# Kernel optimization log

Measured on AMD Instinct MI355X. Metric: run time of the kernel, lower is better.

The kernel has to match this reference:

```python
import jax, jax.numpy as jnp
import numpy as np

K = 256          # num_embeddings
D = 128          # embedding_dim
COMMIT = 0.25
DECAY = 0.99
EPS = 1e-5


def setup_inputs() -> dict:
    key = jax.random.key(0)
    k1, k2, k3 = jax.random.split(key, 3)
    z = jax.random.normal(k1, (128, D, 32, 32), dtype=jnp.float32)
    codebook = jax.random.uniform(k2, (K, D), dtype=jnp.float32, minval=-1.0 / K, maxval=1.0 / K)
    ema_count = jnp.ones((K,), dtype=jnp.float32)
    ema_weight = jax.random.normal(k3, (K, D), dtype=jnp.float32)
    return {"z": z, "codebook": codebook, "ema_count": ema_count, "ema_weight": ema_weight}


def reference(z, codebook, ema_count, ema_weight):
    B, C, H, W = z.shape
    # [B,C,H,W] -> [B*H*W, C]
    z_flat = z.transpose(0, 2, 3, 1).reshape(-1, C)
    N = z_flat.shape[0]

    # squared L2 distances to codebook: [N, K]
    d = (z_flat * z_flat).sum(1, keepdims=True) \
        - 2.0 * (z_flat @ codebook.T) \
        + (codebook * codebook).sum(1)
    idx = jnp.argmin(d, axis=1)                      # [N]

    # codebook lookup (equivalent to one-hot @ codebook, without materializing one-hot)
    quantized_flat = codebook[idx]                   # [N, D]
    quantized = quantized_flat.reshape(B, H, W, C).transpose(0, 3, 1, 2)

    # EMA codebook update (training branch; random unused-entry reset omitted)
    ones = jnp.ones((N,), dtype=z_flat.dtype)
    enc_sum = jax.ops.segment_sum(ones, idx, num_segments=K)          # [K]
    enc_batch = jax.ops.segment_sum(z_flat, idx, num_segments=K)      # [K, D]
    new_count = DECAY * ema_count + (1.0 - DECAY) * enc_sum
    new_weight = DECAY * ema_weight + (1.0 - DECAY) * enc_batch
    n = new_count.sum()
    normalized_count = (new_count + EPS) / (n + K * EPS) * n
    new_codebook = new_weight / normalized_count[:, None]

    # losses
    codebook_loss = jnp.mean((jax.lax.stop_gradient(z) - quantized) ** 2)
    commitment_loss = COMMIT * jnp.mean((jax.lax.stop_gradient(quantized) - z) ** 2)

    # straight-through estimator
    quantized_st = z + jax.lax.stop_gradient(quantized - z)

    return (quantized_st, idx.reshape(B, H, W), commitment_loss, codebook_loss,
            new_codebook, new_count, new_weight)
```

## Files before the change

### kernel.cpp

```cpp
#include <hip/hip_runtime.h>

#define K 256
#define D 128
#define HW 1024
#define CHW 131072
#define N_TOT 131072
#define NELEM 16777216

#define WS_C2 0
#define WS_ENCSUM 256
#define WS_ENCB 512
#define WS_LOSS 33280
#define WS_FLAGCNT 33281
#define WS_LIST 33282
#define FLAG_CAP 16384
#define WS_PART 49666
#define PBLK 64
#define PSTRIDE 33024
#define WS_CBT (WS_PART + PBLK * PSTRIDE)
#define WS_CBH 2195972
#define WS_CBL 2212356

#define OUT_Q 0
#define OUT_IDX 16777216
#define OUT_COMMIT 16908288
#define OUT_CBLOSS 16908289
#define OUT_NEWCB 16908290
#define OUT_NEWCNT 16941058
#define OUT_NEWW 16941314

#define TAU 5e-5f
#define MT 64
#define ZST 68

typedef __attribute__((ext_vector_type(8))) short short8;
typedef __attribute__((ext_vector_type(4))) float floatx4;

__device__ __forceinline__ void cvt_split(const float* xv, short8* hi, short8* lo) {
    union U { uint32_t u[4]; short8 s; } H, L;
    #pragma unroll
    for (int p = 0; p < 4; ++p) {
        uint32_t u0 = __float_as_uint(xv[2 * p]);
        uint32_t u1 = __float_as_uint(xv[2 * p + 1]);
        H.u[p] = (u0 >> 16) | (u1 & 0xFFFF0000u);
        float h0 = __uint_as_float(u0 & 0xFFFF0000u);
        float h1 = __uint_as_float(u1 & 0xFFFF0000u);
        float l0 = xv[2 * p] - h0;
        float l1 = xv[2 * p + 1] - h1;
        L.u[p] = (__float_as_uint(l0) >> 16) | (__float_as_uint(l1) & 0xFFFF0000u);
    }
    *hi = H.s; *lo = L.s;
}

__global__ void k_prep(const float* __restrict__ cb, float* __restrict__ ws) {
    #pragma clang fp contract(off)
    const int blk = blockIdx.x, t = threadIdx.x;
    if (blk == 0) {
        int k = t;
        if (k == 0) { ws[WS_LOSS] = 0.0f; ((int*)ws)[WS_FLAGCNT] = 0; }
        const float* row = cb + (size_t)k * D;
        float r[8];
        #pragma unroll
        for (int j = 0; j < 8; ++j) r[j] = row[j] * row[j];
        for (int i = 8; i < D; i += 8) {
            #pragma unroll
            for (int j = 0; j < 8; ++j) r[j] = r[j] + row[i + j] * row[i + j];
        }
        ws[WS_C2 + k] = ((r[0] + r[1]) + (r[2] + r[3])) + ((r[4] + r[5]) + (r[6] + r[7]));
    } else {
        int e = (blk - 1) * 4 + (t >> 6);
        int lane = t & 63;
        int ds = e >> 4, ktg = e & 15;
        int code = ktg * 16 + (lane & 15);
        int d0 = ds * 32 + (lane >> 4) * 8;
        float xv[8];
        #pragma unroll
        for (int j = 0; j < 8; ++j) xv[j] = cb[(size_t)code * D + d0 + j];
        short8 h, l;
        cvt_split(xv, &h, &l);
        union V { short8 s; uint4 u; } Hv, Lv;
        Hv.s = h; Lv.s = l;
        uint32_t* wsu = (uint32_t*)ws;
        reinterpret_cast<uint4*>(wsu + WS_CBH)[e * 64 + lane] = Hv.u;
        reinterpret_cast<uint4*>(wsu + WS_CBL)[e * 64 + lane] = Lv.u;
    }
}

__global__ void __launch_bounds__(256, 3)
k_main(const float* __restrict__ z, const float* __restrict__ cb,
       float* __restrict__ ws, float* __restrict__ out) {
    __shared__ float zs[D * ZST];
    __shared__ float c2L[K];
    __shared__ float mgB[2][MT];
    __shared__ float mgS[2][MT];
    __shared__ int   mgK[2][MT];
    __shared__ int bkA[MT];
    __shared__ float lsw[4];

    const int t = threadIdx.x;
    const int blk = blockIdx.x;
    const int n0 = blk * MT;
    const int b = n0 >> 10;
    const int hw0 = n0 & 1023;

    c2L[t] = -0.5f * ws[WS_C2 + t];

    {
        const float4* __restrict__ z4 = reinterpret_cast<const float4*>(z);
        const size_t zbase4 = (size_t)b * (CHW / 4) + (hw0 >> 2);
        #pragma unroll
        for (int i = 0; i < 8; ++i) {
            int f = i * 256 + t;
            int dd = f >> 4, n4 = f & 15;
            float4 v = z4[zbase4 + (size_t)dd * (HW / 4) + n4];
            *reinterpret_cast<float4*>(&zs[dd * ZST + 4 * n4]) = v;
        }
    }
    __syncthreads();

    const int lane = t & 63, w = t >> 6;
    const int col = lane & 15, quad = lane >> 4;
    const int kh = w & 1;
    const int mh = w >> 1;

    short8 Ah[2][4], Al[2][4];
    {
        const int rbase = quad * 8 * ZST + mh * 32 + col;
        #pragma unroll
        for (int mt = 0; mt < 2; ++mt)
            #pragma unroll
            for (int ds = 0; ds < 4; ++ds) {
                float xv[8];
                #pragma unroll
                for (int j = 0; j < 8; ++j)
                    xv[j] = zs[rbase + (ds * 32 + j) * ZST + mt * 16];
                cvt_split(xv, &Ah[mt][ds], &Al[mt][ds]);
            }
    }

    const uint32_t* wsu = (const uint32_t*)ws;
    const uint4* __restrict__ bh4 = reinterpret_cast<const uint4*>(wsu + WS_CBH);
    const uint4* __restrict__ bl4 = reinterpret_cast<const uint4*>(wsu + WS_CBL);

    float best[2][4], second[2][4];
    int bk[2][4];
    #pragma unroll
    for (int mt = 0; mt < 2; ++mt)
        #pragma unroll
        for (int r = 0; r < 4; ++r) { best[mt][r] = -3.4e38f; second[mt][r] = -3.4e38f; bk[mt][r] = 0; }

    #pragma unroll
    for (int kt = 0; kt < 8; ++kt) {
        float iv = c2L[kh * 128 + kt * 16 + col];
        floatx4 acc[2];
        #pragma unroll
        for (int mt = 0; mt < 2; ++mt) {
            acc[mt][0] = iv; acc[mt][1] = iv; acc[mt][2] = iv; acc[mt][3] = iv;
        }
        union V { uint4 u; short8 s; } BX[4], BY[4];
        #pragma unroll
        for (int ds = 0; ds < 4; ++ds) {
            int fi = (ds * 16 + kh * 8 + kt) * 64 + lane;
            BX[ds].u = bh4[fi];
            BY[ds].u = bl4[fi];
        }
        #pragma unroll
        for (int ds = 0; ds < 4; ++ds) {
            #pragma unroll
            for (int mt = 0; mt < 2; ++mt) {
                acc[mt] = __builtin_amdgcn_mfma_f32_16x16x32_bf16(Ah[mt][ds], BX[ds].s, acc[mt], 0, 0, 0);
                acc[mt] = __builtin_amdgcn_mfma_f32_16x16x32_bf16(Ah[mt][ds], BY[ds].s, acc[mt], 0, 0, 0);
                acc[mt] = __builtin_amdgcn_mfma_f32_16x16x32_bf16(Al[mt][ds], BX[ds].s, acc[mt], 0, 0, 0);
            }
        }
        int kc = kh * 128 + kt * 16 + col;
        #pragma unroll
        for (int mt = 0; mt < 2; ++mt)
            #pragma unroll
            for (int r = 0; r < 4; ++r) {
                float s = acc[mt][r];
                if (s > best[mt][r]) { second[mt][r] = best[mt][r]; best[mt][r] = s; bk[mt][r] = kc; }
                else if (s > second[mt][r]) second[mt][r] = s;
            }
    }

    #pragma unroll
    for (int off = 1; off < 16; off <<= 1) {
        #pragma unroll
        for (int mt = 0; mt < 2; ++mt)
            #pragma unroll
            for (int r = 0; r < 4; ++r) {
                float ob = __shfl_xor(best[mt][r], off);
                float os = __shfl_xor(second[mt][r], off);
                int ok = __shfl_xor(bk[mt][r], off);
                float nb = fmaxf(best[mt][r], ob);
                float ns = fmaxf(fminf(best[mt][r], ob), fmaxf(second[mt][r], os));
                bk[mt][r] = (ob > best[mt][r]) ? ok : bk[mt][r];
                best[mt][r] = nb; second[mt][r] = ns;
            }
    }

    if (col == 0) {
        #pragma unroll
        for (int mt = 0; mt < 2; ++mt)
            #pragma unroll
            for (int r = 0; r < 4; ++r) {
                int nl = mh * 32 + mt * 16 + quad * 4 + r;
                mgB[kh][nl] = best[mt][r];
                mgS[kh][nl] = second[mt][r];
                mgK[kh][nl] = bk[mt][r];
            }
    }
    __syncthreads();

    if (t < MT) {
        float B1 = mgB[0][t], S = mgS[0][t];
        int KB = mgK[0][t];
        {
            float ob = mgB[1][t], os = mgS[1][t];
            int ok = mgK[1][t];
            float nb = fmaxf(B1, ob);
            float ns = fmaxf(fminf(B1, ob), fmaxf(S, os));
            KB = (ob > B1) ? ok : KB;
            B1 = nb; S = ns;
        }
        int n = n0 + t;
        bool fl = (B1 - S) < TAU;
        if (fl) {
            int slot = atomicAdd((int*)ws + WS_FLAGCNT, 1);
            if (slot < FLAG_CAP) ((int*)ws)[WS_LIST + slot] = n;
            else fl = false;
        }
        if (!fl) { out[OUT_IDX + n] = (float)KB; bkA[t] = KB; }
        else bkA[t] = -1;
    }
    __syncthreads();

    const int nl = t & 63, dp = t >> 6;
    const int bkn = bkA[nl];
    float lsum = 0.0f;
    if (bkn >= 0) {
        const float4* __restrict__ cb4 = reinterpret_cast<const float4*>(cb);
        float* __restrict__ op = out + OUT_Q + (size_t)b * CHW + hw0 + nl;
        #pragma unroll
        for (int u = 0; u < 8; ++u) {
            float4 q4 = cb4[bkn * 32 + dp * 8 + u];
            int d = dp * 32 + u * 4;
            #pragma unroll
            for (int cc = 0; cc < 4; ++cc) {
                float zv = zs[(d + cc) * ZST + nl];
                float q = ((const float*)&q4)[cc];
                op[(size_t)(d + cc) * HW] = zv + (q - zv);
                float tdf = zv - q;
                lsum = fmaf(tdf, tdf, lsum);
            }
        }
    }
    #pragma unroll
    for (int off = 32; off >= 1; off >>= 1) lsum += __shfl_down(lsum, off);
    if ((t & 63) == 0) lsw[w] = lsum;
    __syncthreads();
    if (t == 0) atomicAdd(ws + WS_LOSS, (lsw[0] + lsw[1]) + (lsw[2] + lsw[3]));
}

__global__ void k_fallback(const float* __restrict__ z, const float* __restrict__ cb,
                           float* __restrict__ ws, float* __restrict__ out) {
    #pragma clang fp contract(off)
    const int tid = threadIdx.x;
    __shared__ float zsF[D];
    __shared__ float z2s;
    __shared__ float dvals[K];
    __shared__ int kidx[K];

    int cnt = ((const int*)ws)[WS_FLAGCNT];
    if (cnt > FLAG_CAP) cnt = FLAG_CAP;

    for (int li = blockIdx.x; li < cnt; li += gridDim.x) {
        const int n = ((const int*)ws)[WS_LIST + li];
        const int b = n >> 10;
        const int hw = n & 1023;

        if (tid < D) zsF[tid] = z[(size_t)b * CHW + (size_t)tid * HW + hw];
        __syncthreads();

        if (tid == 0) {
            float r[8];
            #pragma unroll
            for (int j = 0; j < 8; ++j) r[j] = zsF[j] * zsF[j];
            for (int i = 8; i < D; i += 8) {
                #pragma unroll
                for (int j = 0; j < 8; ++j) r[j] = r[j] + zsF[i + j] * zsF[i + j];
            }
            z2s = ((r[0] + r[1]) + (r[2] + r[3])) + ((r[4] + r[5]) + (r[6] + r[7]));
        }
        __syncthreads();

        {
            const float4* __restrict__ row4 =
                reinterpret_cast<const float4*>(cb + (size_t)tid * D);
            double a0 = 0.0, a1 = 0.0, a2 = 0.0, a3 = 0.0;
            #pragma unroll 4
            for (int d4 = 0; d4 < 32; ++d4) {
                float4 cv = row4[d4];
                const float* zz = &zsF[d4 * 4];
                a0 += (double)zz[0] * (double)cv.x;
                a1 += (double)zz[1] * (double)cv.y;
                a2 += (double)zz[2] * (double)cv.z;
                a3 += (double)zz[3] * (double)cv.w;
            }
            float zc = (float)((a0 + a1) + (a2 + a3));
            float dq = (z2s - 2.0f * zc) + ws[WS_C2 + tid];
            dvals[tid] = dq;
            kidx[tid] = tid;
        }
        __syncthreads();

        for (int s = K / 2; s > 0; s >>= 1) {
            if (tid < s) {
                float ov = dvals[tid + s]; int ok = kidx[tid + s];
                float mv = dvals[tid];     int mk2 = kidx[tid];
                if (ov < mv || (ov == mv && ok < mk2)) { dvals[tid] = ov; kidx[tid] = ok; }
            }
            __syncthreads();
        }
        const int bk = kidx[0];
        __syncthreads();

        float t2 = 0.0f;
        if (tid == 0) out[OUT_IDX + n] = (float)bk;
        if (tid < D) {
            float q = cb[(size_t)bk * D + tid];
            out[OUT_Q + (size_t)b * CHW + (size_t)tid * HW + hw] = zsF[tid] + (q - zsF[tid]);
            float t = zsF[tid] - q;
            t2 = t * t;
        }
        dvals[tid] = t2;
        __syncthreads();
        for (int s = K / 2; s > 0; s >>= 1) {
            if (tid < s) dvals[tid] += dvals[tid + s];
            __syncthreads();
        }
        if (tid == 0) atomicAdd(ws + WS_LOSS, dvals[0]);
        __syncthreads();
    }
}

#define GN 2048
__global__ void k_sort(const float* __restrict__ out, float* __restrict__ ws) {
    __shared__ int idxs[GN];
    __shared__ int cnt[K];
    __shared__ int incl[K];
    __shared__ int fill[K];

    const int t = threadIdx.x;
    const int p = blockIdx.x;

    cnt[t] = 0;
    __syncthreads();
    for (int j = t; j < GN; j += 256) {
        int k = (int)out[OUT_IDX + (size_t)p * GN + j];
        idxs[j] = k;
        atomicAdd(&cnt[k], 1);
    }
    __syncthreads();
    incl[t] = cnt[t];
    __syncthreads();
    for (int off = 1; off < K; off <<= 1) {
        int v = incl[t];
        if (t >= off) v += incl[t - off];
        __syncthreads();
        incl[t] = v;
        __syncthreads();
    }
    const int st = incl[t] - cnt[t];
    fill[t] = st;
    ((int*)ws)[WS_LIST + p * K + t] = (st << 16) | cnt[t];
    ws[WS_PART + (size_t)p * PSTRIDE + K * D + t] = (float)cnt[t];
    __syncthreads();

    unsigned short* ord = (unsigned short*)(ws + WS_CBT);
    for (int j = t; j < GN; j += 256) {
        int k = idxs[j];
        int pos = atomicAdd(&fill[k], 1);
        ord[p * GN + pos] = (unsigned short)j;
    }
}

#define GZST 2052
__global__ void __launch_bounds__(1024, 4)
k_gather(const float* __restrict__ z, float* __restrict__ ws) {
    __shared__ float zsg[8 * GZST];
    __shared__ unsigned short ords[GN];
    __shared__ int skc[K];

    const int t = threadIdx.x;
    const int p = blockIdx.x >> 4;
    const int c = blockIdx.x & 15;

    const unsigned short* ord = (const unsigned short*)(ws + WS_CBT);
    for (int j = t; j < GN; j += 1024) ords[j] = ord[p * GN + j];
    if (t < K) skc[t] = ((const int*)ws)[WS_LIST + p * K + t];

    const float4* __restrict__ z4 = reinterpret_cast<const float4*>(z);
    for (int j = t; j < 8 * 512; j += 1024) {
        int d2 = j >> 9, n4 = j & 511;
        int bb = n4 >> 8, hw4 = n4 & 255;
        float4 v = z4[(size_t)(2 * p + bb) * (CHW / 4)
                      + (size_t)(c * 8 + d2) * (HW / 4) + hw4];
        *reinterpret_cast<float4*>(&zsg[d2 * GZST + 4 * n4]) = v;
    }
    __syncthreads();

    const int dl = t & 7;
    const int k0 = (t >> 3) * 2;
    float* __restrict__ pout = ws + WS_PART + (size_t)p * PSTRIDE;
    const float* __restrict__ zrow = zsg + dl * GZST;
    #pragma unroll
    for (int kk = 0; kk < 2; ++kk) {
        int k = k0 + kk;
        int sc = skc[k];
        int s = sc >> 16, e = s + (sc & 0xFFFF);
        float a = 0.0f;
        for (int q = s; q < e; ++q) a += zrow[ords[q]];
        pout[(size_t)k * D + c * 8 + dl] = a;
    }
}

__global__ void k_emareduce(float* __restrict__ ws) {
    int e = blockIdx.x * 256 + threadIdx.x;
    if (e >= PSTRIDE) return;
    const float* __restrict__ p = ws + WS_PART + e;
    float s = 0.0f;
    #pragma unroll 8
    for (int g = 0; g < PBLK; ++g) s += p[(size_t)g * PSTRIDE];
    if (e < K * D) ws[WS_ENCB + e] = s;
    else ws[WS_ENCSUM + (e - K * D)] = s;
}

__global__ void k_finalize(const float* __restrict__ ema_count,
                           const float* __restrict__ ema_weight,
                           const float* __restrict__ ws, float* __restrict__ out) {
    #pragma clang fp contract(off)
    const int tid = threadIdx.x;
    const int blk = blockIdx.x;
    __shared__ float red[K];
    __shared__ float normc[K];

    const float DEC = 0.99f;
    const float OMD = (float)(1.0 - 0.99);

    float nc = DEC * ema_count[tid] + OMD * ws[WS_ENCSUM + tid];
    red[tid] = nc;
    __syncthreads();
    for (int s = K / 2; s > 0; s >>= 1) {
        if (tid < s) red[tid] += red[tid + s];
        __syncthreads();
    }
    const float nt = red[0];
    normc[tid] = (nc + 1e-5f) / (nt + 0.00256f) * nt;
    __syncthreads();

    if (blk == 0) {
        out[OUT_NEWCNT + tid] = nc;
        if (tid == 0) {
            float m = ws[WS_LOSS] / 16777216.0f;
            out[OUT_CBLOSS] = m;
            out[OUT_COMMIT] = 0.25f * m;
        }
    }

    const int i = blk * 256 + tid;
    const int k = i >> 7;
    float nw = DEC * ema_weight[i] + OMD * ws[WS_ENCB + i];
    out[OUT_NEWW + i] = nw;
    out[OUT_NEWCB + i] = nw / normc[k];
}

extern "C" void kernel_launch(void* const* d_in, const int* in_sizes, int n_in,
                              void* d_out, int out_size, void* d_ws, size_t ws_size,
                              hipStream_t stream) {
    const float* z = (const float*)d_in[0];
    const float* cb = (const float*)d_in[1];
    const float* ema_count = (const float*)d_in[2];
    const float* ema_weight = (const float*)d_in[3];
    float* out = (float*)d_out;
    float* ws = (float*)d_ws;

    k_prep<<<17, 256, 0, stream>>>(cb, ws);
    k_main<<<N_TOT / MT, 256, 0, stream>>>(z, cb, ws, out);
    k_fallback<<<2048, 256, 0, stream>>>(z, cb, ws, out);
    k_sort<<<64, 256, 0, stream>>>(out, ws);
    k_gather<<<1024, 1024, 0, stream>>>(z, ws);
    k_emareduce<<<129, 256, 0, stream>>>(ws);
    k_finalize<<<128, 256, 0, stream>>>(ema_count, ema_weight, ws, out);
}
```

Before: 229.0 us.

## Fuse EMA partial reduction into finalize, widen sort blocks, raise main occupancy

Removes the separate k_emareduce kernel and has k_finalize sum the 64 per-group partials directly, saving a launch and a round-trip through workspace. Each finalize block now re-reads all 64 count partials for the 256 codes, which adds redundant reads. Separately, k_sort runs with 1024 threads instead of 256, k_fallback gets twice as many blocks, and k_main's launch bounds ask for 4 blocks per CU, which may cause register spills.

```diff
diff --git a/kernel.cpp b/kernel.cpp
--- a/kernel.cpp
+++ b/kernel.cpp
@@ -86,7 +86,7 @@
     }
 }
 
-__global__ void __launch_bounds__(256, 3)
+__global__ void __launch_bounds__(256, 4)
 k_main(const float* __restrict__ z, const float* __restrict__ cb,
        float* __restrict__ ws, float* __restrict__ out) {
     __shared__ float zs[D * ZST];
@@ -355,31 +355,33 @@
     const int t = threadIdx.x;
     const int p = blockIdx.x;
 
-    cnt[t] = 0;
-    __syncthreads();
-    for (int j = t; j < GN; j += 256) {
+    if (t < K) cnt[t] = 0;
+    __syncthreads();
+    for (int j = t; j < GN; j += 1024) {
         int k = (int)out[OUT_IDX + (size_t)p * GN + j];
         idxs[j] = k;
         atomicAdd(&cnt[k], 1);
     }
     __syncthreads();
-    incl[t] = cnt[t];
+    if (t < K) incl[t] = cnt[t];
     __syncthreads();
     for (int off = 1; off < K; off <<= 1) {
-        int v = incl[t];
-        if (t >= off) v += incl[t - off];
-        __syncthreads();
-        incl[t] = v;
-        __syncthreads();
-    }
-    const int st = incl[t] - cnt[t];
-    fill[t] = st;
-    ((int*)ws)[WS_LIST + p * K + t] = (st << 16) | cnt[t];
-    ws[WS_PART + (size_t)p * PSTRIDE + K * D + t] = (float)cnt[t];
+        int v = 0;
+        if (t < K) { v = incl[t]; if (t >= off) v += incl[t - off]; }
+        __syncthreads();
+        if (t < K) incl[t] = v;
+        __syncthreads();
+    }
+    if (t < K) {
+        const int st = incl[t] - cnt[t];
+        fill[t] = st;
+        ((int*)ws)[WS_LIST + p * K + t] = (st << 16) | cnt[t];
+        ws[WS_PART + (size_t)p * PSTRIDE + K * D + t] = (float)cnt[t];
+    }
     __syncthreads();
 
     unsigned short* ord = (unsigned short*)(ws + WS_CBT);
-    for (int j = t; j < GN; j += 256) {
+    for (int j = t; j < GN; j += 1024) {
         int k = idxs[j];
         int pos = atomicAdd(&fill[k], 1);
         ord[p * GN + pos] = (unsigned short)j;
@@ -424,17 +426,6 @@
         for (int q = s; q < e; ++q) a += zrow[ords[q]];
         pout[(size_t)k * D + c * 8 + dl] = a;
     }
-}
-
-__global__ void k_emareduce(float* __restrict__ ws) {
-    int e = blockIdx.x * 256 + threadIdx.x;
-    if (e >= PSTRIDE) return;
-    const float* __restrict__ p = ws + WS_PART + e;
-    float s = 0.0f;
-    #pragma unroll 8
-    for (int g = 0; g < PBLK; ++g) s += p[(size_t)g * PSTRIDE];
-    if (e < K * D) ws[WS_ENCB + e] = s;
-    else ws[WS_ENCSUM + (e - K * D)] = s;
 }
 
 __global__ void k_finalize(const float* __restrict__ ema_count,
@@ -449,7 +440,13 @@
     const float DEC = 0.99f;
     const float OMD = (float)(1.0 - 0.99);
 
-    float nc = DEC * ema_count[tid] + OMD * ws[WS_ENCSUM + tid];
+    float es = 0.0f;
+    {
+        const float* __restrict__ ps = ws + WS_PART + K * D + tid;
+        #pragma unroll 8
+        for (int g = 0; g < PBLK; ++g) es += ps[(size_t)g * PSTRIDE];
+    }
+    float nc = DEC * ema_count[tid] + OMD * es;
     red[tid] = nc;
     __syncthreads();
     for (int s = K / 2; s > 0; s >>= 1) {
@@ -470,8 +467,14 @@
     }
 
     const int i = blk * 256 + tid;
+    float eb = 0.0f;
+    {
+        const float* __restrict__ pb = ws + WS_PART + i;
+        #pragma unroll 8
+        for (int g = 0; g < PBLK; ++g) eb += pb[(size_t)g * PSTRIDE];
+    }
     const int k = i >> 7;
-    float nw = DEC * ema_weight[i] + OMD * ws[WS_ENCB + i];
+    float nw = DEC * ema_weight[i] + OMD * eb;
     out[OUT_NEWW + i] = nw;
     out[OUT_NEWCB + i] = nw / normc[k];
 }
@@ -488,9 +491,8 @@
 
     k_prep<<<17, 256, 0, stream>>>(cb, ws);
     k_main<<<N_TOT / MT, 256, 0, stream>>>(z, cb, ws, out);
-    k_fallback<<<2048, 256, 0, stream>>>(z, cb, ws, out);
-    k_sort<<<64, 256, 0, stream>>>(out, ws);
+    k_fallback<<<4096, 256, 0, stream>>>(z, cb, ws, out);
+    k_sort<<<64, 1024, 0, stream>>>(out, ws);
     k_gather<<<1024, 1024, 0, stream>>>(z, ws);
-    k_emareduce<<<129, 256, 0, stream>>>(ws);
     k_finalize<<<128, 256, 0, stream>>>(ema_count, ema_weight, ws, out);
 }
```

New measurement: 227.3 us. About the same (-0.8%).
